# Kernel optimization log

Measured on AMD Instinct MI355X. Metric: run time of the kernel, lower is better.

The kernel has to match this reference:

```python
import jax, jax.numpy as jnp
import numpy as np

EPS = 0.05
N_ITER = 50
IN_DIM = 4096
PROJ_DIM = 128
BATCH = 4096


def sinkhorn_loss(x, y, eps=EPS, n_iter=N_ITER):
    # x, y: [B, N, D]
    B, N, _ = x.shape
    # squared euclidean cost, matches torch.cdist(p=2).pow(2): [B, N, N]
    C = jnp.sum((x[:, :, None, :] - y[:, None, :, :]) ** 2, axis=-1)
    log_K = -C / eps
    log_ab = -jnp.log(jnp.asarray(N, x.dtype))  # log_a = log_b = -log N
    log_u0 = jnp.zeros((B, N), x.dtype)
    log_v0 = jnp.zeros((B, N), x.dtype)

    def step(carry, _):
        log_u, log_v = carry
        log_u = log_ab - jax.scipy.special.logsumexp(log_K + log_v[:, None, :], axis=-1)
        log_v = log_ab - jax.scipy.special.logsumexp(log_K + log_u[:, :, None], axis=-2)
        return (log_u, log_v), None

    (log_u, log_v), _ = jax.lax.scan(step, (log_u0, log_v0), None, length=n_iter)
    log_T = log_K + log_u[:, :, None] + log_v[:, None, :]
    T = jnp.exp(log_T)
    transport_cost = jnp.sum(T * C, axis=(1, 2))
    entropic = eps * jnp.sum(T * (log_T - 1.0), axis=(1, 2))
    return jnp.mean(transport_cost + entropic)


def setup_inputs() -> dict:
    key = jax.random.key(0)
    ks = jax.random.split(key, 6)
    scale = 1.0 / np.sqrt(IN_DIM)
    return {
        "x_ct": jax.random.normal(ks[0], (BATCH, IN_DIM), jnp.float32),
        "x_txt": jax.random.normal(ks[1], (BATCH, IN_DIM), jnp.float32),
        "x_lab": jax.random.normal(ks[2], (BATCH, IN_DIM), jnp.float32),
        "W_ct": jax.random.uniform(ks[3], (PROJ_DIM, IN_DIM), jnp.float32, -scale, scale),
        "W_txt": jax.random.uniform(ks[4], (PROJ_DIM, IN_DIM), jnp.float32, -scale, scale),
        "W_lab": jax.random.uniform(ks[5], (PROJ_DIM, IN_DIM), jnp.float32, -scale, scale),
    }


def reference(x_ct, x_txt, x_lab, W_ct, W_txt, W_lab):
    # Linear projections (no bias): z = x @ W.T -> [B, P]
    z_ct = x_ct @ W_ct.T
    z_txt = x_txt @ W_txt.T
    z_lab = x_lab @ W_lab.T
    # unsqueeze(1): each becomes a point cloud of N=1 points
    z_ct_e = z_ct[:, None, :]
    z_txt_e = z_txt[:, None, :]
    z_lab_e = z_lab[:, None, :]
    loss_ct_txt = sinkhorn_loss(z_ct_e, z_txt_e)
    loss_ct_lab = sinkhorn_loss(z_ct_e, z_lab_e)
    loss_txt_lab = sinkhorn_loss(z_txt_e, z_lab_e)
    ot_loss = (loss_ct_txt + loss_ct_lab + loss_txt_lab) / 3.0
    aligned = (z_ct + z_txt + z_lab) / 3.0
    return (aligned, ot_loss)
```

## Files before the change

kernel.cpp:

```cpp
#include <hip/hip_runtime.h>
#include <stdint.h>

typedef __attribute__((ext_vector_type(8))) short short8;
typedef __attribute__((ext_vector_type(4))) float f32x4;
typedef __attribute__((ext_vector_type(4))) uint32_t u32x4;

#define K_DIM 4096
#define N_DIM 128
#define M_DIM 4096
#define MN ((size_t)M_DIM * N_DIM)
#define NS 4
#define BK 32
#define NTI 32
#define FRAG_PER_SLAB MN

__device__ __forceinline__ uint16_t f2bf(float f) {
    uint32_t u = __float_as_uint(f);
    return (uint16_t)((u + 0x7FFFu + ((u >> 16) & 1u)) >> 16);
}
__device__ __forceinline__ float bf2f(uint16_t h) {
    return __uint_as_float((uint32_t)h << 16);
}

__device__ __forceinline__ short8 cvt8(const float4 lo, const float4 hi) {
    short8 r;
    r[0] = (short)f2bf(lo.x); r[1] = (short)f2bf(lo.y);
    r[2] = (short)f2bf(lo.z); r[3] = (short)f2bf(lo.w);
    r[4] = (short)f2bf(hi.x); r[5] = (short)f2bf(hi.y);
    r[6] = (short)f2bf(hi.z); r[7] = (short)f2bf(hi.w);
    return r;
}

__global__ __launch_bounds__(256) void prep_kernel(
    const float* __restrict__ W0, const float* __restrict__ W1,
    const float* __restrict__ W2, uint16_t* __restrict__ Wb)
{
    int gid = blockIdx.x * 256 + threadIdx.x;
    int g = gid >> 16;
    int e = (gid & 65535) * 8;
    const float* W = (g == 0) ? W0 : (g == 1) ? W1 : W2;
    float4 lo = *(const float4*)(W + e);
    float4 hi = *(const float4*)(W + e + 4);
    *(short8*)(Wb + (size_t)g * (N_DIM * K_DIM) + e) = cvt8(lo, hi);
}

__global__ __launch_bounds__(256, 3) void gemm3_kernel(
    const float* __restrict__ x0, const float* __restrict__ x1,
    const float* __restrict__ x2, const uint16_t* __restrict__ Wb,
    uint16_t* __restrict__ zpart)
{
    __shared__ uint16_t lds[4][4096];

    const int tid  = threadIdx.x;
    const int lane = tid & 63;
    const int wv   = tid >> 6;

    const int lid = (blockIdx.x & 7) * 96 + (blockIdx.x >> 3);
    const int g   = lid >> 8;
    const int rem = lid & 255;
    const int ks  = rem >> 6;
    const int mt  = rem & 63;
    const int k0  = ks * (K_DIM / NS);

    const float* x = (g == 0) ? x0 : (g == 1) ? x1 : x2;
    const uint16_t* Wg = Wb + (size_t)g * (N_DIM * K_DIM);

    const int c16 = lane & 15;
    const int qg  = lane >> 4;
    const int rowbase = mt * 64 + wv * 16;
    const float* aptr = x + (size_t)(rowbase + c16) * K_DIM + qg * 8 + k0;

    const uint16_t* wsrc0;
    const uint16_t* wsrc1;
    {
        const int e0 = tid * 8, e1 = 2048 + tid * 8;
        const int col0 = e0 >> 5, s0 = (e0 >> 3) & 3;
        const int col1 = e1 >> 5, s1 = (e1 >> 3) & 3;
        wsrc0 = Wg + (size_t)col0 * K_DIM + (s0 ^ ((col0 >> 1) & 3)) * 8 + k0;
        wsrc1 = Wg + (size_t)col1 * K_DIM + (s1 ^ ((col1 >> 1) & 3)) * 8 + k0;
    }

    const int cswz = (c16 >> 1) & 3;
    const int sswz = (qg ^ cswz) * 8;

    f32x4 acc[8];
#pragma unroll
    for (int nf = 0; nf < 8; ++nf) acc[nf] = (f32x4)0.f;

    float4 areg[4][2];

#define STAGE(B, KB) do {                                                      \
    __builtin_amdgcn_global_load_lds(                                          \
        (const __attribute__((address_space(1))) uint32_t*)(wsrc0 + (KB)),     \
        (__attribute__((address_space(3))) uint32_t*)&lds[B][wv * 512],        \
        16, 0, 0);                                                             \
    __builtin_amdgcn_global_load_lds(                                          \
        (const __attribute__((address_space(1))) uint32_t*)(wsrc1 + (KB)),     \
        (__attribute__((address_space(3))) uint32_t*)&lds[B][2048 + wv * 512], \
        16, 0, 0);                                                             \
  } while (0)

#define BATCH(B, KB) do {                                                      \
    STAGE(B, KB);                                                              \
    areg[B][0] = *(const float4*)(aptr + (KB));                                \
    areg[B][1] = *(const float4*)(aptr + (KB) + 4);                            \
  } while (0)

#define ITER(SLOT, KT, VM, ISSUE) do {                                         \
    asm volatile("s_waitcnt lgkmcnt(0)" ::: "memory");                         \
    asm volatile("s_barrier" ::: "memory");                                    \
    if (ISSUE) { BATCH((((SLOT) + 2) & 3), (((KT) + 2) * BK)); }               \
    asm volatile("s_waitcnt vmcnt(%0)" :: "i"(VM) : "memory");                 \
    {                                                                          \
        short8 af = cvt8(areg[SLOT][0], areg[SLOT][1]);                        \
        _Pragma("unroll")                                                      \
        for (int nf = 0; nf < 8; ++nf) {                                       \
            short8 bf = *(const short8*)&lds[SLOT][(nf * 16 + c16) * 32 + sswz]; \
            acc[nf] = __builtin_amdgcn_mfma_f32_16x16x32_bf16(af, bf, acc[nf], 0, 0, 0); \
        }                                                                      \
    }                                                                          \
  } while (0)

    BATCH(0, 0);
    BATCH(1, BK);

#pragma unroll
    for (int kt = 0; kt < 28; kt += 4) {
        ITER(0, kt + 0, 8, true);
        ITER(1, kt + 1, 8, true);
        ITER(2, kt + 2, 8, true);
        ITER(3, kt + 3, 8, true);
    }
    ITER(0, 28, 8, true);
    ITER(1, 29, 8, true);
    ITER(2, 30, 4, false);
    ITER(3, 31, 0, false);

#undef ITER
#undef BATCH
#undef STAGE

    uint32_t dw[16];
#pragma unroll
    for (int nf = 0; nf < 8; ++nf) {
        dw[nf * 2]     = (uint32_t)f2bf(acc[nf][0]) | ((uint32_t)f2bf(acc[nf][1]) << 16);
        dw[nf * 2 + 1] = (uint32_t)f2bf(acc[nf][2]) | ((uint32_t)f2bf(acc[nf][3]) << 16);
    }
    uint16_t* zp = zpart + (size_t)(ks * 3 + g) * FRAG_PER_SLAB
                 + (size_t)mt * 8192 + (size_t)(wv * 64 + lane) * 32;
    uint32_t* zp32 = (uint32_t*)zp;
#pragma unroll
    for (int j = 0; j < 4; ++j) {
        u32x4 v = { dw[j * 4], dw[j * 4 + 1], dw[j * 4 + 2], dw[j * 4 + 3] };
        *(u32x4*)(zp32 + j * 4) = v;
    }
}

__global__ __launch_bounds__(256) void combine_kernel(
    const uint16_t* __restrict__ zpart, float* __restrict__ out,
    float* __restrict__ partials)
{
    const int tid  = threadIdx.x;
    const int gtid = blockIdx.x * 256 + tid;
    const size_t F0 = (size_t)gtid * 8;

    const int idx_base = (int)(F0 & 31);
    const int lane = (int)((F0 >> 5) & 63);
    const int wv   = (int)((F0 >> 11) & 3);
    const int mt   = (int)(F0 >> 13);
    const int c16  = lane & 15;
    const int qg   = lane >> 4;
    const int rowb = mt * 64 + wv * 16 + qg * 4;

    float zs[3][8];
#pragma unroll
    for (int g = 0; g < 3; ++g)
#pragma unroll
        for (int v = 0; v < 8; ++v) zs[g][v] = 0.f;

#pragma unroll
    for (int ks = 0; ks < NS; ++ks) {
#pragma unroll
        for (int g = 0; g < 3; ++g) {
            const short8 pv = *(const short8*)(zpart + (size_t)(ks * 3 + g) * FRAG_PER_SLAB + F0);
#pragma unroll
            for (int v = 0; v < 8; ++v) zs[g][v] += bf2f((uint16_t)pv[v]);
        }
    }

    float s = 0.f;
#pragma unroll
    for (int v = 0; v < 8; ++v) {
        const float a = zs[0][v], b = zs[1][v], c = zs[2][v];
        const int idx = idx_base + v;
        const int nf = idx >> 2, r = idx & 3;
        out[(size_t)(rowb + r) * N_DIM + nf * 16 + c16] = (a + b + c) * (1.f / 3.f);
        const float d1 = a - b, d2 = a - c, d3 = b - c;
        s += d1 * d1 + d2 * d2 + d3 * d3;
    }

#pragma unroll
    for (int off = 32; off > 0; off >>= 1) s += __shfl_xor(s, off);
    __shared__ float wsum[4];
    if ((tid & 63) == 0) wsum[tid >> 6] = s;
    __syncthreads();
    if (tid == 0) partials[blockIdx.x] = wsum[0] + wsum[1] + wsum[2] + wsum[3];
}

__global__ __launch_bounds__(256) void finalize_kernel(
    const float* __restrict__ partials, float* __restrict__ out)
{
    const int tid = threadIdx.x;
    float s = partials[tid];
#pragma unroll
    for (int off = 32; off > 0; off >>= 1) s += __shfl_xor(s, off);
    __shared__ float wsum[4];
    if ((tid & 63) == 0) wsum[tid >> 6] = s;
    __syncthreads();
    if (tid == 0)
        out[MN] = (wsum[0] + wsum[1] + wsum[2] + wsum[3]) * (1.f / 12288.f) - 0.05f;
}

extern "C" void kernel_launch(void* const* d_in, const int* in_sizes, int n_in,
                              void* d_out, int out_size, void* d_ws, size_t ws_size,
                              hipStream_t stream)
{
    const float* x0 = (const float*)d_in[0];
    const float* x1 = (const float*)d_in[1];
    const float* x2 = (const float*)d_in[2];
    const float* W0 = (const float*)d_in[3];
    const float* W1 = (const float*)d_in[4];
    const float* W2 = (const float*)d_in[5];
    float* out = (float*)d_out;

    const size_t zpart_bytes = (size_t)NS * 3 * FRAG_PER_SLAB * sizeof(uint16_t);
    const size_t wb_bytes    = (size_t)3 * N_DIM * K_DIM * sizeof(uint16_t);

    char* ws = (char*)d_ws;
    uint16_t* zpart    = (uint16_t*)ws;
    uint16_t* Wb       = (uint16_t*)(ws + zpart_bytes);
    float*    partials = (float*)(ws + zpart_bytes + wb_bytes);

    prep_kernel    <<<768, 256, 0, stream>>>(W0, W1, W2, Wb);
    gemm3_kernel   <<<768, 256, 0, stream>>>(x0, x1, x2, Wb, zpart);
    combine_kernel <<<256, 256, 0, stream>>>(zpart, out, partials);
    finalize_kernel<<<  1, 256, 0, stream>>>(partials, out);
}
```

Before: 55.19 us.

## Double K-tile to 64 and switch to triple-buffered LDS pipeline

Raises the K step per iteration from 32 to 64, halving the number of barrier/waitcnt iterations and issuing four async W loads plus four A float4 loads per stage. Replaces the 4-slot ring with a 3-slot ring of twice the size, with a new 8-way XOR swizzle for the wider rows and adjusted vmcnt thresholds. The aim is to amortize synchronization overhead and give more MFMA work between barriers. In exchange, LDS use grows from 32KB to 48KB and more registers are held for A, which may reduce occupancy under launch_bounds(256,3).

Measured after the change: 51.92 us, median of 2. -5.9%, faster.

```diff
diff --git a/kernel.cpp b/kernel.cpp
--- a/kernel.cpp
+++ b/kernel.cpp
@@ -10,8 +10,7 @@
 #define M_DIM 4096
 #define MN ((size_t)M_DIM * N_DIM)
 #define NS 4
-#define BK 32
-#define NTI 32
+#define BK 64
 #define FRAG_PER_SLAB MN
 
 __device__ __forceinline__ uint16_t f2bf(float f) {
@@ -49,7 +48,7 @@
     const float* __restrict__ x2, const uint16_t* __restrict__ Wb,
     uint16_t* __restrict__ zpart)
 {
-    __shared__ uint16_t lds[4][4096];
+    __shared__ uint16_t lds[3][8192];
 
     const int tid  = threadIdx.x;
     const int lane = tid & 63;
@@ -70,52 +69,50 @@
     const int rowbase = mt * 64 + wv * 16;
     const float* aptr = x + (size_t)(rowbase + c16) * K_DIM + qg * 8 + k0;
 
-    const uint16_t* wsrc0;
-    const uint16_t* wsrc1;
-    {
-        const int e0 = tid * 8, e1 = 2048 + tid * 8;
-        const int col0 = e0 >> 5, s0 = (e0 >> 3) & 3;
-        const int col1 = e1 >> 5, s1 = (e1 >> 3) & 3;
-        wsrc0 = Wg + (size_t)col0 * K_DIM + (s0 ^ ((col0 >> 1) & 3)) * 8 + k0;
-        wsrc1 = Wg + (size_t)col1 * K_DIM + (s1 ^ ((col1 >> 1) & 3)) * 8 + k0;
-    }
-
-    const int cswz = (c16 >> 1) & 3;
-    const int sswz = (qg ^ cswz) * 8;
+    const int t8 = tid >> 3, slot = tid & 7;
+    const uint16_t* wsrc[4];
+#pragma unroll
+    for (int c = 0; c < 4; ++c) {
+        int col = c * 32 + t8;
+        wsrc[c] = Wg + (size_t)col * K_DIM + (slot ^ (col & 7)) * 8 + k0;
+    }
 
     f32x4 acc[8];
 #pragma unroll
     for (int nf = 0; nf < 8; ++nf) acc[nf] = (f32x4)0.f;
 
-    float4 areg[4][2];
+    float4 areg[3][4];
 
 #define STAGE(B, KB) do {                                                      \
-    __builtin_amdgcn_global_load_lds(                                          \
-        (const __attribute__((address_space(1))) uint32_t*)(wsrc0 + (KB)),     \
-        (__attribute__((address_space(3))) uint32_t*)&lds[B][wv * 512],        \
-        16, 0, 0);                                                             \
-    __builtin_amdgcn_global_load_lds(                                          \
-        (const __attribute__((address_space(1))) uint32_t*)(wsrc1 + (KB)),     \
-        (__attribute__((address_space(3))) uint32_t*)&lds[B][2048 + wv * 512], \
-        16, 0, 0);                                                             \
+    _Pragma("unroll")                                                          \
+    for (int c = 0; c < 4; ++c) {                                              \
+        __builtin_amdgcn_global_load_lds(                                      \
+            (const __attribute__((address_space(1))) uint32_t*)(wsrc[c] + (KB)), \
+            (__attribute__((address_space(3))) uint32_t*)&lds[B][c * 2048 + wv * 512], \
+            16, 0, 0);                                                         \
+    }                                                                          \
   } while (0)
 
 #define BATCH(B, KB) do {                                                      \
     STAGE(B, KB);                                                              \
     areg[B][0] = *(const float4*)(aptr + (KB));                                \
     areg[B][1] = *(const float4*)(aptr + (KB) + 4);                            \
+    areg[B][2] = *(const float4*)(aptr + (KB) + 32);                           \
+    areg[B][3] = *(const float4*)(aptr + (KB) + 36);                           \
   } while (0)
 
 #define ITER(SLOT, KT, VM, ISSUE) do {                                         \
     asm volatile("s_waitcnt lgkmcnt(0)" ::: "memory");                         \
     asm volatile("s_barrier" ::: "memory");                                    \
-    if (ISSUE) { BATCH((((SLOT) + 2) & 3), (((KT) + 2) * BK)); }               \
+    if (ISSUE) { BATCH((((SLOT) + 2) % 3), (((KT) + 2) * BK)); }               \
     asm volatile("s_waitcnt vmcnt(%0)" :: "i"(VM) : "memory");                 \
-    {                                                                          \
-        short8 af = cvt8(areg[SLOT][0], areg[SLOT][1]);                        \
+    _Pragma("unroll")                                                          \
+    for (int h = 0; h < 2; ++h) {                                              \
+        short8 af = cvt8(areg[SLOT][2 * h], areg[SLOT][2 * h + 1]);            \
+        const int boff = c16 * 64 + (((h * 4) + qg) ^ (lane & 7)) * 8;         \
         _Pragma("unroll")                                                      \
         for (int nf = 0; nf < 8; ++nf) {                                       \
-            short8 bf = *(const short8*)&lds[SLOT][(nf * 16 + c16) * 32 + sswz]; \
+            short8 bf = *(const short8*)&lds[SLOT][nf * 1024 + boff];          \
             acc[nf] = __builtin_amdgcn_mfma_f32_16x16x32_bf16(af, bf, acc[nf], 0, 0, 0); \
         }                                                                      \
     }                                                                          \
@@ -125,16 +122,15 @@
     BATCH(1, BK);
 
 #pragma unroll
-    for (int kt = 0; kt < 28; kt += 4) {
-        ITER(0, kt + 0, 8, true);
-        ITER(1, kt + 1, 8, true);
-        ITER(2, kt + 2, 8, true);
-        ITER(3, kt + 3, 8, true);
-    }
-    ITER(0, 28, 8, true);
-    ITER(1, 29, 8, true);
-    ITER(2, 30, 4, false);
-    ITER(3, 31, 0, false);
+    for (int kt = 0; kt < 12; kt += 3) {
+        ITER(0, kt + 0, 16, true);
+        ITER(1, kt + 1, 16, true);
+        ITER(2, kt + 2, 16, true);
+    }
+    ITER(0, 12, 16, true);
+    ITER(1, 13, 16, true);
+    ITER(2, 14,  8, false);
+    ITER(0, 15,  0, false);
 
 #undef ITER
 #undef BATCH
```
